# Kernel tuning notes

Hardware: AMD Instinct MI355X
Metric: run time of the kernel (lower is better)

Reference implementation:

```python
import jax, jax.numpy as jnp
import numpy as np

N_NODES = 10000
N_EDGES = 640000
D = 128


def setup_inputs() -> dict:
    key = jax.random.key(0)
    ks = jax.random.split(key, 8)
    x = jax.random.normal(ks[0], (N_NODES, D), dtype=jnp.float32)
    edge_weight = jax.random.uniform(ks[1], (N_EDGES,), dtype=jnp.float32)
    W0 = jax.random.normal(ks[2], (D, D), dtype=jnp.float32) * (1.0 / np.sqrt(D))
    b0 = jnp.zeros((D,), dtype=jnp.float32)
    W1 = jax.random.normal(ks[3], (D, D), dtype=jnp.float32) * (1.0 / np.sqrt(D))
    b1 = jnp.zeros((D,), dtype=jnp.float32)
    src = jax.random.randint(ks[4], (N_EDGES,), 0, N_NODES)
    dst = jax.random.randint(ks[5], (N_EDGES,), 0, N_NODES)
    return {"x": x, "edge_weight": edge_weight, "W0": W0, "b0": b0,
            "W1": W1, "b1": b1, "src": src, "dst": dst}


def _graph_conv(h, src, dst, edge_weight, W, b):
    # DGL GraphConv with norm='both', bias, activation=relu.
    n = h.shape[0]
    ones = jnp.ones((src.shape[0],), dtype=h.dtype)
    out_deg = jax.ops.segment_sum(ones, src, num_segments=n)
    in_deg = jax.ops.segment_sum(ones, dst, num_segments=n)
    norm_src = jax.lax.rsqrt(jnp.maximum(out_deg, 1.0))  # [N]
    norm_dst = jax.lax.rsqrt(jnp.maximum(in_deg, 1.0))   # [N]
    h = h * norm_src[:, None]
    # gather -> weight edges -> scatter-add (sparse neighbor aggregation)
    msg = h[src] * edge_weight[:, None]                  # [E, D]
    agg = jax.ops.segment_sum(msg, dst, num_segments=n)  # [N, D]
    rst = agg @ W                                        # in_feats == out_feats: aggregate first
    rst = rst * norm_dst[:, None] + b
    return jax.nn.relu(rst)  # activation inside GraphConv


def reference(x, edge_weight, W0, b0, W1, b1, src, dst):
    # NET.forward (full-graph path): per layer GraphConv -> activation -> dropout.
    # Dropout is identity in eval mode; outer relu after GraphConv's internal relu is idempotent
    # but applied for faithfulness.
    h = jax.nn.relu(_graph_conv(x, src, dst, edge_weight, W0, b0))
    h = jax.nn.relu(_graph_conv(h, src, dst, edge_weight, W1, b1))
    return h  # predict is None (n_classes=None)
```

## Files before the change

kernel.cpp:

```cpp
#include <hip/hip_runtime.h>
#include <hip/hip_fp16.h>

#define D 128
#define NB 256
#define Q 8
#define BQ (NB / Q)
#define NBINS_MAX 10016
#define GM 32

__global__ __launch_bounds__(256) void cast_kernel(const float* __restrict__ x, __half* __restrict__ xh, int total4) {
    int i = blockIdx.x * 256 + threadIdx.x;
    if (i >= total4) return;
    float4 v = *(const float4*)(x + (size_t)i * 4);
    __half2 a = __floats2half2_rn(v.x, v.y);
    __half2 b = __floats2half2_rn(v.z, v.w);
    *(__half2*)(xh + (size_t)i * 4) = a;
    *(__half2*)(xh + (size_t)i * 4 + 2) = b;
}

__global__ __launch_bounds__(256) void hist_kernel(const int* __restrict__ src, const int* __restrict__ dst,
                                                   int* __restrict__ pd, unsigned short* __restrict__ ps,
                                                   int E, int n) {
    __shared__ __align__(16) int hd[NBINS_MAX];
    __shared__ __align__(16) int hs[NBINS_MAX];
    int b = blockIdx.x, t = threadIdx.x;
    int chunk = (E + NB - 1) / NB;
    int e0 = b * chunk, e1 = min(e0 + chunk, E);
    int nq = (n + 3) >> 2;
    for (int i = t; i < nq; i += 256) {
        *(int4*)(&hd[i * 4]) = make_int4(0, 0, 0, 0);
        *(int4*)(&hs[i * 4]) = make_int4(0, 0, 0, 0);
    }
    __syncthreads();
    for (int e = e0 + t; e < e1; e += 256) {
        atomicAdd(&hd[dst[e]], 1);
        atomicAdd(&hs[src[e]], 1);
    }
    __syncthreads();
    int nf = n >> 2;
    for (int i = t; i < nf; i += 256) {
        int4 h = *(const int4*)(&hd[i * 4]);
        *(int4*)(pd + (size_t)b * n + i * 4) = h;
        int4 s = *(const int4*)(&hs[i * 4]);
        uint2 u;
        u.x = (unsigned)(s.x & 0xFFFF) | ((unsigned)(s.y & 0xFFFF) << 16);
        u.y = (unsigned)(s.z & 0xFFFF) | ((unsigned)(s.w & 0xFFFF) << 16);
        *(uint2*)(ps + (size_t)b * n + i * 4) = u;
    }
    for (int i = nf * 4 + t; i < n; i += 256) {
        pd[(size_t)b * n + i] = hd[i];
        ps[(size_t)b * n + i] = (unsigned short)hs[i];
    }
}

__global__ __launch_bounds__(256) void colscan_kernel(int* __restrict__ pd, const unsigned short* __restrict__ ps,
                                                      int* __restrict__ qtot_d, int* __restrict__ qtot_s, int n) {
    int bin4 = (blockIdx.x * 256 + threadIdx.x) * 4;
    int q = blockIdx.y;
    if (bin4 >= n) return;
    int b0 = q * BQ;
    if (bin4 + 3 < n) {
        int4 run = make_int4(0, 0, 0, 0);
        int4 ssum = make_int4(0, 0, 0, 0);
#pragma unroll 8
        for (int j = 0; j < BQ; ++j) {
            size_t idx = (size_t)(b0 + j) * n + bin4;
            int4 v = *(const int4*)(pd + idx);
            *(int4*)(pd + idx) = run;
            run.x += v.x; run.y += v.y; run.z += v.z; run.w += v.w;
            uint2 u = *(const uint2*)(ps + idx);
            ssum.x += (int)(u.x & 0xFFFF); ssum.y += (int)(u.x >> 16);
            ssum.z += (int)(u.y & 0xFFFF); ssum.w += (int)(u.y >> 16);
        }
        *(int4*)(qtot_d + (size_t)q * n + bin4) = run;
        *(int4*)(qtot_s + (size_t)q * n + bin4) = ssum;
    } else {
        for (int bin = bin4; bin < n; ++bin) {
            int run = 0, ssum = 0;
            for (int j = 0; j < BQ; ++j) {
                size_t idx = (size_t)(b0 + j) * n + bin;
                int v = pd[idx];
                pd[idx] = run;
                run += v;
                ssum += (int)ps[idx];
            }
            qtot_d[(size_t)q * n + bin] = run;
            qtot_s[(size_t)q * n + bin] = ssum;
        }
    }
}

__global__ __launch_bounds__(256) void finalize_kernel(int* __restrict__ qtot_d ,
                                                       const int* __restrict__ qtot_s,
                                                       int* __restrict__ in_deg,
                                                       float* __restrict__ norm_src, float* __restrict__ norm_dst,
                                                       int n) {
    int b4 = (blockIdx.x * 256 + threadIdx.x) * 4;
    if (b4 >= n) return;
    if (b4 + 3 < n) {
        int4 qv[Q];
#pragma unroll
        for (int q = 0; q < Q; ++q) qv[q] = *(const int4*)(qtot_d + (size_t)q * n + b4);
        int4 run = make_int4(0, 0, 0, 0);
#pragma unroll
        for (int q = 0; q < Q; ++q) {
            *(int4*)(qtot_d + (size_t)q * n + b4) = run;
            run.x += qv[q].x; run.y += qv[q].y; run.z += qv[q].z; run.w += qv[q].w;
        }
        *(int4*)(in_deg + b4) = run;
        norm_dst[b4 + 0] = rsqrtf(fmaxf((float)run.x, 1.0f));
        norm_dst[b4 + 1] = rsqrtf(fmaxf((float)run.y, 1.0f));
        norm_dst[b4 + 2] = rsqrtf(fmaxf((float)run.z, 1.0f));
        norm_dst[b4 + 3] = rsqrtf(fmaxf((float)run.w, 1.0f));
        int4 st = make_int4(0, 0, 0, 0);
#pragma unroll
        for (int q = 0; q < Q; ++q) {
            int4 v = *(const int4*)(qtot_s + (size_t)q * n + b4);
            st.x += v.x; st.y += v.y; st.z += v.z; st.w += v.w;
        }
        norm_src[b4 + 0] = rsqrtf(fmaxf((float)st.x, 1.0f));
        norm_src[b4 + 1] = rsqrtf(fmaxf((float)st.y, 1.0f));
        norm_src[b4 + 2] = rsqrtf(fmaxf((float)st.z, 1.0f));
        norm_src[b4 + 3] = rsqrtf(fmaxf((float)st.w, 1.0f));
    } else {
        for (int bin = b4; bin < n; ++bin) {
            int run = 0;
            for (int q = 0; q < Q; ++q) {
                size_t i = (size_t)q * n + bin;
                int v = qtot_d[i];
                qtot_d[i] = run;
                run += v;
            }
            in_deg[bin] = run;
            norm_dst[bin] = rsqrtf(fmaxf((float)run, 1.0f));
            int tot = 0;
            for (int q = 0; q < Q; ++q) tot += qtot_s[(size_t)q * n + bin];
            norm_src[bin] = rsqrtf(fmaxf((float)tot, 1.0f));
        }
    }
}

__global__ __launch_bounds__(1024) void scan_kernel(const int* __restrict__ in_deg, int* __restrict__ row_start, int n) {
    __shared__ int buf[NBINS_MAX];
    __shared__ int part[1024];
    int t = threadIdx.x;
    for (int i = t; i < n; i += 1024) buf[i] = in_deg[i];
    __syncthreads();
    int ipt = (n + 1023) / 1024;
    int lo = min(t * ipt, n), hi = min(lo + ipt, n);
    int s = 0;
    for (int i = lo; i < hi; ++i) s += buf[i];
    part[t] = s;
    __syncthreads();
    for (int off = 1; off < 1024; off <<= 1) {
        int v = 0;
        if (t >= off) v = part[t - off];
        __syncthreads();
        if (t >= off) part[t] += v;
        __syncthreads();
    }
    int run = part[t] - s;
    for (int i = lo; i < hi; ++i) {
        int v = buf[i];
        buf[i] = run;
        run += v;
    }
    __syncthreads();
    for (int i = t; i < n; i += 1024) row_start[i] = buf[i];
    if (t == 0) row_start[n] = part[1023];
}

__global__ __launch_bounds__(256) void fill_kernel(const int* __restrict__ src, const int* __restrict__ dst,
                                                   const float* __restrict__ ew, const float* __restrict__ ns,
                                                   const int* __restrict__ row_start, const int* __restrict__ qbase,
                                                   const int* __restrict__ pd,
                                                   int2* __restrict__ sorted, int E, int n) {
    __shared__ __align__(16) int cursor[NBINS_MAX];
    int b = blockIdx.x, t = threadIdx.x;
    int q = b / BQ;
    int chunk = (E + NB - 1) / NB;
    int e0 = b * chunk, e1 = min(e0 + chunk, E);
    int nf = n >> 2;
    for (int i = t; i < nf; i += 256) {
        int4 r = *(const int4*)(row_start + i * 4);
        int4 a = *(const int4*)(qbase + (size_t)q * n + i * 4);
        int4 c = *(const int4*)(pd + (size_t)b * n + i * 4);
        *(int4*)(&cursor[i * 4]) = make_int4(r.x + a.x + c.x, r.y + a.y + c.y,
                                             r.z + a.z + c.z, r.w + a.w + c.w);
    }
    for (int i = nf * 4 + t; i < n; i += 256)
        cursor[i] = row_start[i] + qbase[(size_t)q * n + i] + pd[(size_t)b * n + i];
    __syncthreads();
    for (int e = e0 + t; e < e1; e += 256) {
        int d = dst[e];
        int slot = atomicAdd(&cursor[d], 1);
        int s = src[e];
        int2 rec;
        rec.x = s;
        rec.y = __float_as_int(ew[e] * ns[s]);
        sorted[slot] = rec;
    }
}

__global__ __launch_bounds__(256) void agg_kernel(const __half* __restrict__ h, const int* __restrict__ row_start,
                                                  const int2* __restrict__ sorted, float* __restrict__ out,
                                                  int n, int qn) {
    int slot  = blockIdx.x & 7;
    int g     = blockIdx.x >> 3;
    int chunk = slot >> 2;
    int quad  = slot & 3;
    int wave  = threadIdx.x >> 6;
    int lane  = threadIdx.x & 63;
    int node  = quad * qn + g * 4 + wave;
    int hiN   = min((quad + 1) * qn, n);
    if (node >= hiN) return;
    const __half* hc = h + chunk * 64 + lane;
    int beg = __builtin_amdgcn_readfirstlane(row_start[node]);
    int end = __builtin_amdgcn_readfirstlane(row_start[node + 1]);
    float acc = 0.f;
    int s = beg;
    if (s < end && (s & 1)) {
        int2 rr = sorted[s];
        acc = fmaf(__int_as_float(rr.y), __half2float(hc[(size_t)rr.x << 7]), acc);
        ++s;
    }
    int4 p0, p1, p2, p3, p4, p5, p6, p7;
    if (s + 16 <= end) {
        p0 = *(const int4*)(sorted + s);
        p1 = *(const int4*)(sorted + s + 2);
        p2 = *(const int4*)(sorted + s + 4);
        p3 = *(const int4*)(sorted + s + 6);
        p4 = *(const int4*)(sorted + s + 8);
        p5 = *(const int4*)(sorted + s + 10);
        p6 = *(const int4*)(sorted + s + 12);
        p7 = *(const int4*)(sorted + s + 14);
    }
    for (; s + 32 <= end; s += 16) {
        int4 q0 = *(const int4*)(sorted + s + 16);
        int4 q1 = *(const int4*)(sorted + s + 18);
        int4 q2 = *(const int4*)(sorted + s + 20);
        int4 q3 = *(const int4*)(sorted + s + 22);
        int4 q4 = *(const int4*)(sorted + s + 24);
        int4 q5 = *(const int4*)(sorted + s + 26);
        int4 q6 = *(const int4*)(sorted + s + 28);
        int4 q7 = *(const int4*)(sorted + s + 30);
        __half x0  = hc[(size_t)p0.x << 7];
        __half x1  = hc[(size_t)p0.z << 7];
        __half x2  = hc[(size_t)p1.x << 7];
        __half x3  = hc[(size_t)p1.z << 7];
        __half x4  = hc[(size_t)p2.x << 7];
        __half x5  = hc[(size_t)p2.z << 7];
        __half x6  = hc[(size_t)p3.x << 7];
        __half x7  = hc[(size_t)p3.z << 7];
        __half x8  = hc[(size_t)p4.x << 7];
        __half x9  = hc[(size_t)p4.z << 7];
        __half x10 = hc[(size_t)p5.x << 7];
        __half x11 = hc[(size_t)p5.z << 7];
        __half x12 = hc[(size_t)p6.x << 7];
        __half x13 = hc[(size_t)p6.z << 7];
        __half x14 = hc[(size_t)p7.x << 7];
        __half x15 = hc[(size_t)p7.z << 7];
        acc = fmaf(__int_as_float(p0.y), __half2float(x0),  acc);
        acc = fmaf(__int_as_float(p0.w), __half2float(x1),  acc);
        acc = fmaf(__int_as_float(p1.y), __half2float(x2),  acc);
        acc = fmaf(__int_as_float(p1.w), __half2float(x3),  acc);
        acc = fmaf(__int_as_float(p2.y), __half2float(x4),  acc);
        acc = fmaf(__int_as_float(p2.w), __half2float(x5),  acc);
        acc = fmaf(__int_as_float(p3.y), __half2float(x6),  acc);
        acc = fmaf(__int_as_float(p3.w), __half2float(x7),  acc);
        acc = fmaf(__int_as_float(p4.y), __half2float(x8),  acc);
        acc = fmaf(__int_as_float(p4.w), __half2float(x9),  acc);
        acc = fmaf(__int_as_float(p5.y), __half2float(x10), acc);
        acc = fmaf(__int_as_float(p5.w), __half2float(x11), acc);
        acc = fmaf(__int_as_float(p6.y), __half2float(x12), acc);
        acc = fmaf(__int_as_float(p6.w), __half2float(x13), acc);
        acc = fmaf(__int_as_float(p7.y), __half2float(x14), acc);
        acc = fmaf(__int_as_float(p7.w), __half2float(x15), acc);
        p0 = q0; p1 = q1; p2 = q2; p3 = q3;
        p4 = q4; p5 = q5; p6 = q6; p7 = q7;
    }
    if (s + 16 <= end) {
        acc = fmaf(__int_as_float(p0.y), __half2float(hc[(size_t)p0.x << 7]), acc);
        acc = fmaf(__int_as_float(p0.w), __half2float(hc[(size_t)p0.z << 7]), acc);
        acc = fmaf(__int_as_float(p1.y), __half2float(hc[(size_t)p1.x << 7]), acc);
        acc = fmaf(__int_as_float(p1.w), __half2float(hc[(size_t)p1.z << 7]), acc);
        acc = fmaf(__int_as_float(p2.y), __half2float(hc[(size_t)p2.x << 7]), acc);
        acc = fmaf(__int_as_float(p2.w), __half2float(hc[(size_t)p2.z << 7]), acc);
        acc = fmaf(__int_as_float(p3.y), __half2float(hc[(size_t)p3.x << 7]), acc);
        acc = fmaf(__int_as_float(p3.w), __half2float(hc[(size_t)p3.z << 7]), acc);
        acc = fmaf(__int_as_float(p4.y), __half2float(hc[(size_t)p4.x << 7]), acc);
        acc = fmaf(__int_as_float(p4.w), __half2float(hc[(size_t)p4.z << 7]), acc);
        acc = fmaf(__int_as_float(p5.y), __half2float(hc[(size_t)p5.x << 7]), acc);
        acc = fmaf(__int_as_float(p5.w), __half2float(hc[(size_t)p5.z << 7]), acc);
        acc = fmaf(__int_as_float(p6.y), __half2float(hc[(size_t)p6.x << 7]), acc);
        acc = fmaf(__int_as_float(p6.w), __half2float(hc[(size_t)p6.z << 7]), acc);
        acc = fmaf(__int_as_float(p7.y), __half2float(hc[(size_t)p7.x << 7]), acc);
        acc = fmaf(__int_as_float(p7.w), __half2float(hc[(size_t)p7.z << 7]), acc);
        s += 16;
    }
    if (s + 8 <= end) {
        int4 a0 = *(const int4*)(sorted + s);
        int4 a1 = *(const int4*)(sorted + s + 2);
        int4 a2 = *(const int4*)(sorted + s + 4);
        int4 a3 = *(const int4*)(sorted + s + 6);
        acc = fmaf(__int_as_float(a0.y), __half2float(hc[(size_t)a0.x << 7]), acc);
        acc = fmaf(__int_as_float(a0.w), __half2float(hc[(size_t)a0.z << 7]), acc);
        acc = fmaf(__int_as_float(a1.y), __half2float(hc[(size_t)a1.x << 7]), acc);
        acc = fmaf(__int_as_float(a1.w), __half2float(hc[(size_t)a1.z << 7]), acc);
        acc = fmaf(__int_as_float(a2.y), __half2float(hc[(size_t)a2.x << 7]), acc);
        acc = fmaf(__int_as_float(a2.w), __half2float(hc[(size_t)a2.z << 7]), acc);
        acc = fmaf(__int_as_float(a3.y), __half2float(hc[(size_t)a3.x << 7]), acc);
        acc = fmaf(__int_as_float(a3.w), __half2float(hc[(size_t)a3.z << 7]), acc);
        s += 8;
    }
    for (; s + 2 <= end; s += 2) {
        int4 p = *(const int4*)(sorted + s);
        acc = fmaf(__int_as_float(p.y), __half2float(hc[(size_t)p.x << 7]), acc);
        acc = fmaf(__int_as_float(p.w), __half2float(hc[(size_t)p.z << 7]), acc);
    }
    if (s < end) {
        int2 rr = sorted[s];
        acc = fmaf(__int_as_float(rr.y), __half2float(hc[(size_t)rr.x << 7]), acc);
    }
    out[((size_t)node << 7) + chunk * 64 + lane] = acc;
}

template <int HALF_OUT>
__global__ __launch_bounds__(256) void gemm_kernel(const float* __restrict__ A, const float* __restrict__ W,
                                                   const float* __restrict__ bias, const float* __restrict__ norm_dst,
                                                   float* __restrict__ out, __half* __restrict__ out_h, int n) {
    __shared__ __align__(16) float sAT[D][GM + 2];
    int tid = threadIdx.x;
    int row0 = blockIdx.x * GM;
    for (int i = tid; i < GM * 32; i += 256) {
        int r = i >> 5;
        int kq = i & 31;
        int rr = row0 + r;
        float4 v = make_float4(0.f, 0.f, 0.f, 0.f);
        if (rr < n) v = *(const float4*)(A + (size_t)rr * D + kq * 4);
        sAT[kq * 4 + 0][r] = v.x;
        sAT[kq * 4 + 1][r] = v.y;
        sAT[kq * 4 + 2][r] = v.z;
        sAT[kq * 4 + 3][r] = v.w;
    }
    __syncthreads();
    int tx = tid & 15;
    int ty = tid >> 4;
    int c0 = tx * 8;
    int r0 = ty * 2;
    float acc0[8], acc1[8];
#pragma unroll
    for (int j = 0; j < 8; ++j) { acc0[j] = 0.f; acc1[j] = 0.f; }
    const float* Wk = W + c0;
#pragma unroll 4
    for (int k = 0; k < D; ++k) {
        float2 a = *(const float2*)&sAT[k][r0];
        float4 w0 = *(const float4*)(Wk);
        float4 w1 = *(const float4*)(Wk + 4);
        Wk += D;
        acc0[0] = fmaf(a.x, w0.x, acc0[0]);
        acc0[1] = fmaf(a.x, w0.y, acc0[1]);
        acc0[2] = fmaf(a.x, w0.z, acc0[2]);
        acc0[3] = fmaf(a.x, w0.w, acc0[3]);
        acc0[4] = fmaf(a.x, w1.x, acc0[4]);
        acc0[5] = fmaf(a.x, w1.y, acc0[5]);
        acc0[6] = fmaf(a.x, w1.z, acc0[6]);
        acc0[7] = fmaf(a.x, w1.w, acc0[7]);
        acc1[0] = fmaf(a.y, w0.x, acc1[0]);
        acc1[1] = fmaf(a.y, w0.y, acc1[1]);
        acc1[2] = fmaf(a.y, w0.z, acc1[2]);
        acc1[3] = fmaf(a.y, w0.w, acc1[3]);
        acc1[4] = fmaf(a.y, w1.x, acc1[4]);
        acc1[5] = fmaf(a.y, w1.y, acc1[5]);
        acc1[6] = fmaf(a.y, w1.z, acc1[6]);
        acc1[7] = fmaf(a.y, w1.w, acc1[7]);
    }
#pragma unroll 2
    for (int rr = 0; rr < 2; ++rr) {
        int r = row0 + r0 + rr;
        if (r >= n) continue;
        float* acc = rr ? acc1 : acc0;
        float nd = norm_dst[r];
        float o[8];
#pragma unroll
        for (int j = 0; j < 8; ++j) o[j] = fmaxf(fmaf(acc[j], nd, bias[c0 + j]), 0.f);
        if (HALF_OUT) {
            __half2 h0 = __floats2half2_rn(o[0], o[1]);
            __half2 h1 = __floats2half2_rn(o[2], o[3]);
            __half2 h2 = __floats2half2_rn(o[4], o[5]);
            __half2 h3 = __floats2half2_rn(o[6], o[7]);
            __half* p = out_h + (size_t)r * D + c0;
            *(__half2*)(p + 0) = h0;
            *(__half2*)(p + 2) = h1;
            *(__half2*)(p + 4) = h2;
            *(__half2*)(p + 6) = h3;
        } else {
            float4 o0 = make_float4(o[0], o[1], o[2], o[3]);
            float4 o1 = make_float4(o[4], o[5], o[6], o[7]);
            *(float4*)(out + (size_t)r * D + c0) = o0;
            *(float4*)(out + (size_t)r * D + c0 + 4) = o1;
        }
    }
}

extern "C" void kernel_launch(void* const* d_in, const int* in_sizes, int n_in,
                              void* d_out, int out_size, void* d_ws, size_t ws_size,
                              hipStream_t stream) {
    const float* x  = (const float*)d_in[0];
    const float* ew = (const float*)d_in[1];
    const float* W0 = (const float*)d_in[2];
    const float* b0 = (const float*)d_in[3];
    const float* W1 = (const float*)d_in[4];
    const float* b1 = (const float*)d_in[5];
    const int* src  = (const int*)d_in[6];
    const int* dst  = (const int*)d_in[7];
    float* out = (float*)d_out;

    int n = in_sizes[0] / D;
    int E = in_sizes[6];
    if (n <= 0 || E <= 0) return;

    char* ws = (char*)d_ws;
    size_t off = 0;
    auto alloc = [&](size_t bytes) -> void* {
        void* p = ws + off;
        off = (off + bytes + 255) & ~(size_t)255;
        return p;
    };
    int* row_start  = (int*)alloc(((size_t)n + 1) * 4);
    int* in_deg     = (int*)alloc((size_t)n * 4);
    float* norm_src = (float*)alloc((size_t)n * 4);
    float* norm_dst = (float*)alloc((size_t)n * 4);
    int* qtot_d     = (int*)alloc((size_t)Q * n * 4);
    int* qtot_s     = (int*)alloc((size_t)Q * n * 4);
    int2* sorted    = (int2*)alloc((size_t)E * 8);
    int* pd         = (int*)alloc((size_t)NB * n * 4);
    unsigned short* ps = (unsigned short*)alloc((size_t)NB * n * 2);
    float* B1       = (float*)alloc((size_t)n * D * 4);
    __half* xh      = (__half*)alloc((size_t)n * D * 2);
    __half* B2h     = (__half*)alloc((size_t)n * D * 2);

    int nb4 = (n + 1023) / 1024;
    int qn = (n + 3) / 4;
    int ab = 8 * ((qn + 3) / 4);
    int gb = (n + GM - 1) / GM;
    int cb = ((n * D / 4) + 255) / 256;

    cast_kernel<<<cb, 256, 0, stream>>>(x, xh, n * D / 4);
    hist_kernel<<<NB, 256, 0, stream>>>(src, dst, pd, ps, E, n);
    colscan_kernel<<<dim3(nb4, Q), 256, 0, stream>>>(pd, ps, qtot_d, qtot_s, n);
    finalize_kernel<<<nb4, 256, 0, stream>>>(qtot_d, qtot_s, in_deg, norm_src, norm_dst, n);
    scan_kernel<<<1, 1024, 0, stream>>>(in_deg, row_start, n);
    fill_kernel<<<NB, 256, 0, stream>>>(src, dst, ew, norm_src, row_start, qtot_d, pd, sorted, E, n);

    agg_kernel<<<ab, 256, 0, stream>>>(xh, row_start, sorted, B1, n, qn);
    gemm_kernel<1><<<gb, 256, 0, stream>>>(B1, W0, b0, norm_dst, nullptr, B2h, n);
    agg_kernel<<<ab, 256, 0, stream>>>(B2h, row_start, sorted, B1, n, qn);
    gemm_kernel<0><<<gb, 256, 0, stream>>>(B1, W1, b1, norm_dst, out, nullptr, n);
}
```

Baseline: 189.4 us.

## Fuse cast into histogram, merge finalize with scan, widen aggregation to half2

Folds the fp32-to-fp16 cast of x into the histogram kernel and merges the finalize and scan kernels into a single 1024-thread block, cutting two launches and the in_deg round-trip. The aggregation kernel now has one wave handle all 128 features of a node using half2 loads, instead of eight blocks splitting each node into 64-column chunks. Each edge record is then read once per node rather than twice, and the gathers are wider. In exchange, finalize work is serialized into one block, and the quad-based node interleaving that may have helped load balance is dropped.

```diff
diff --git a/kernel.cpp b/kernel.cpp
--- a/kernel.cpp
+++ b/kernel.cpp
@@ -8,22 +8,20 @@
 #define NBINS_MAX 10016
 #define GM 32
 
-__global__ __launch_bounds__(256) void cast_kernel(const float* __restrict__ x, __half* __restrict__ xh, int total4) {
-    int i = blockIdx.x * 256 + threadIdx.x;
-    if (i >= total4) return;
-    float4 v = *(const float4*)(x + (size_t)i * 4);
-    __half2 a = __floats2half2_rn(v.x, v.y);
-    __half2 b = __floats2half2_rn(v.z, v.w);
-    *(__half2*)(xh + (size_t)i * 4) = a;
-    *(__half2*)(xh + (size_t)i * 4 + 2) = b;
-}
-
 __global__ __launch_bounds__(256) void hist_kernel(const int* __restrict__ src, const int* __restrict__ dst,
+                                                   const float* __restrict__ x, __half* __restrict__ xh, int total4,
                                                    int* __restrict__ pd, unsigned short* __restrict__ ps,
                                                    int E, int n) {
     __shared__ __align__(16) int hd[NBINS_MAX];
     __shared__ __align__(16) int hs[NBINS_MAX];
     int b = blockIdx.x, t = threadIdx.x;
+    for (int i = b * 256 + t; i < total4; i += NB * 256) {
+        float4 v = *(const float4*)(x + (size_t)i * 4);
+        __half2 a = __floats2half2_rn(v.x, v.y);
+        __half2 c = __floats2half2_rn(v.z, v.w);
+        *(__half2*)(xh + (size_t)i * 4) = a;
+        *(__half2*)(xh + (size_t)i * 4 + 2) = c;
+    }
     int chunk = (E + NB - 1) / NB;
     int e0 = b * chunk, e1 = min(e0 + chunk, E);
     int nq = (n + 3) >> 2;
@@ -90,66 +88,61 @@
     }
 }
 
-__global__ __launch_bounds__(256) void finalize_kernel(int* __restrict__ qtot_d ,
-                                                       const int* __restrict__ qtot_s,
-                                                       int* __restrict__ in_deg,
+__global__ __launch_bounds__(1024) void finscan_kernel(int* __restrict__ qtot_d, const int* __restrict__ qtot_s,
+                                                       int* __restrict__ row_start,
                                                        float* __restrict__ norm_src, float* __restrict__ norm_dst,
                                                        int n) {
-    int b4 = (blockIdx.x * 256 + threadIdx.x) * 4;
-    if (b4 >= n) return;
-    if (b4 + 3 < n) {
-        int4 qv[Q];
-#pragma unroll
-        for (int q = 0; q < Q; ++q) qv[q] = *(const int4*)(qtot_d + (size_t)q * n + b4);
-        int4 run = make_int4(0, 0, 0, 0);
-#pragma unroll
-        for (int q = 0; q < Q; ++q) {
-            *(int4*)(qtot_d + (size_t)q * n + b4) = run;
-            run.x += qv[q].x; run.y += qv[q].y; run.z += qv[q].z; run.w += qv[q].w;
-        }
-        *(int4*)(in_deg + b4) = run;
-        norm_dst[b4 + 0] = rsqrtf(fmaxf((float)run.x, 1.0f));
-        norm_dst[b4 + 1] = rsqrtf(fmaxf((float)run.y, 1.0f));
-        norm_dst[b4 + 2] = rsqrtf(fmaxf((float)run.z, 1.0f));
-        norm_dst[b4 + 3] = rsqrtf(fmaxf((float)run.w, 1.0f));
-        int4 st = make_int4(0, 0, 0, 0);
-#pragma unroll
-        for (int q = 0; q < Q; ++q) {
-            int4 v = *(const int4*)(qtot_s + (size_t)q * n + b4);
-            st.x += v.x; st.y += v.y; st.z += v.z; st.w += v.w;
-        }
-        norm_src[b4 + 0] = rsqrtf(fmaxf((float)st.x, 1.0f));
-        norm_src[b4 + 1] = rsqrtf(fmaxf((float)st.y, 1.0f));
-        norm_src[b4 + 2] = rsqrtf(fmaxf((float)st.z, 1.0f));
-        norm_src[b4 + 3] = rsqrtf(fmaxf((float)st.w, 1.0f));
-    } else {
-        for (int bin = b4; bin < n; ++bin) {
-            int run = 0;
-            for (int q = 0; q < Q; ++q) {
-                size_t i = (size_t)q * n + bin;
-                int v = qtot_d[i];
-                qtot_d[i] = run;
-                run += v;
-            }
-            in_deg[bin] = run;
-            norm_dst[bin] = rsqrtf(fmaxf((float)run, 1.0f));
-            int tot = 0;
-            for (int q = 0; q < Q; ++q) tot += qtot_s[(size_t)q * n + bin];
-            norm_src[bin] = rsqrtf(fmaxf((float)tot, 1.0f));
-        }
-    }
-}
-
-__global__ __launch_bounds__(1024) void scan_kernel(const int* __restrict__ in_deg, int* __restrict__ row_start, int n) {
-    __shared__ int buf[NBINS_MAX];
+    __shared__ int deg[NBINS_MAX];
     __shared__ int part[1024];
     int t = threadIdx.x;
-    for (int i = t; i < n; i += 1024) buf[i] = in_deg[i];
+    for (int b4 = t * 4; b4 < n; b4 += 4096) {
+        if (b4 + 3 < n) {
+            int4 qv[Q];
+#pragma unroll
+            for (int q = 0; q < Q; ++q) qv[q] = *(const int4*)(qtot_d + (size_t)q * n + b4);
+            int4 run = make_int4(0, 0, 0, 0);
+#pragma unroll
+            for (int q = 0; q < Q; ++q) {
+                *(int4*)(qtot_d + (size_t)q * n + b4) = run;
+                run.x += qv[q].x; run.y += qv[q].y; run.z += qv[q].z; run.w += qv[q].w;
+            }
+            *(int4*)(&deg[b4]) = run;
+            norm_dst[b4 + 0] = rsqrtf(fmaxf((float)run.x, 1.0f));
+            norm_dst[b4 + 1] = rsqrtf(fmaxf((float)run.y, 1.0f));
+            norm_dst[b4 + 2] = rsqrtf(fmaxf((float)run.z, 1.0f));
+            norm_dst[b4 + 3] = rsqrtf(fmaxf((float)run.w, 1.0f));
+            int4 st = make_int4(0, 0, 0, 0);
+#pragma unroll
+            for (int q = 0; q < Q; ++q) {
+                int4 v = *(const int4*)(qtot_s + (size_t)q * n + b4);
+                st.x += v.x; st.y += v.y; st.z += v.z; st.w += v.w;
+            }
+            norm_src[b4 + 0] = rsqrtf(fmaxf((float)st.x, 1.0f));
+            norm_src[b4 + 1] = rsqrtf(fmaxf((float)st.y, 1.0f));
+            norm_src[b4 + 2] = rsqrtf(fmaxf((float)st.z, 1.0f));
+            norm_src[b4 + 3] = rsqrtf(fmaxf((float)st.w, 1.0f));
+        } else {
+            for (int bin = b4; bin < n; ++bin) {
+                int run = 0;
+                for (int q = 0; q < Q; ++q) {
+                    size_t i = (size_t)q * n + bin;
+                    int v = qtot_d[i];
+                    qtot_d[i] = run;
+                    run += v;
+                }
+                deg[bin] = run;
+                norm_dst[bin] = rsqrtf(fmaxf((float)run, 1.0f));
+                int tot = 0;
+                for (int q = 0; q < Q; ++q) tot += qtot_s[(size_t)q * n + bin];
+                norm_src[bin] = rsqrtf(fmaxf((float)tot, 1.0f));
+            }
+        }
+    }
     __syncthreads();
     int ipt = (n + 1023) / 1024;
     int lo = min(t * ipt, n), hi = min(lo + ipt, n);
     int s = 0;
-    for (int i = lo; i < hi; ++i) s += buf[i];
+    for (int i = lo; i < hi; ++i) s += deg[i];
     part[t] = s;
     __syncthreads();
     for (int off = 1; off < 1024; off <<= 1) {
@@ -161,13 +154,11 @@
     }
     int run = part[t] - s;
     for (int i = lo; i < hi; ++i) {
-        int v = buf[i];
-        buf[i] = run;
+        int v = deg[i];
+        row_start[i] = run;
         run += v;
     }
-    __syncthreads();
-    for (int i = t; i < n; i += 1024) row_start[i] = buf[i];
-    if (t == 0) row_start[n] = part[1023];
+    if (t == 1023) row_start[n] = part[1023];
 }
 
 __global__ __launch_bounds__(256) void fill_kernel(const int* __restrict__ src, const int* __restrict__ dst,
@@ -203,25 +194,21 @@
 }
 
 __global__ __launch_bounds__(256) void agg_kernel(const __half* __restrict__ h, const int* __restrict__ row_start,
-                                                  const int2* __restrict__ sorted, float* __restrict__ out,
-                                                  int n, int qn) {
-    int slot  = blockIdx.x & 7;
-    int g     = blockIdx.x >> 3;
-    int chunk = slot >> 2;
-    int quad  = slot & 3;
-    int wave  = threadIdx.x >> 6;
-    int lane  = threadIdx.x & 63;
-    int node  = quad * qn + g * 4 + wave;
-    int hiN   = min((quad + 1) * qn, n);
-    if (node >= hiN) return;
-    const __half* hc = h + chunk * 64 + lane;
+                                                  const int2* __restrict__ sorted, float* __restrict__ out, int n) {
+    int wave = threadIdx.x >> 6;
+    int lane = threadIdx.x & 63;
+    int node = blockIdx.x * 4 + wave;
+    if (node >= n) return;
+    const __half2* hc = (const __half2*)h + lane;
     int beg = __builtin_amdgcn_readfirstlane(row_start[node]);
     int end = __builtin_amdgcn_readfirstlane(row_start[node + 1]);
-    float acc = 0.f;
+    float accx = 0.f, accy = 0.f;
     int s = beg;
     if (s < end && (s & 1)) {
         int2 rr = sorted[s];
-        acc = fmaf(__int_as_float(rr.y), __half2float(hc[(size_t)rr.x << 7]), acc);
+        float w = __int_as_float(rr.y);
+        float2 f = __half22float2(hc[(size_t)rr.x << 6]);
+        accx = fmaf(w, f.x, accx); accy = fmaf(w, f.y, accy);
         ++s;
     }
     int4 p0, p1, p2, p3, p4, p5, p6, p7;
@@ -244,58 +231,60 @@
         int4 q5 = *(const int4*)(sorted + s + 26);
         int4 q6 = *(const int4*)(sorted + s + 28);
         int4 q7 = *(const int4*)(sorted + s + 30);
-        __half x0  = hc[(size_t)p0.x << 7];
-        __half x1  = hc[(size_t)p0.z << 7];
-        __half x2  = hc[(size_t)p1.x << 7];
-        __half x3  = hc[(size_t)p1.z << 7];
-        __half x4  = hc[(size_t)p2.x << 7];
-        __half x5  = hc[(size_t)p2.z << 7];
-        __half x6  = hc[(size_t)p3.x << 7];
-        __half x7  = hc[(size_t)p3.z << 7];
-        __half x8  = hc[(size_t)p4.x << 7];
-        __half x9  = hc[(size_t)p4.z << 7];
-        __half x10 = hc[(size_t)p5.x << 7];
-        __half x11 = hc[(size_t)p5.z << 7];
-        __half x12 = hc[(size_t)p6.x << 7];
-        __half x13 = hc[(size_t)p6.z << 7];
-        __half x14 = hc[(size_t)p7.x << 7];
-        __half x15 = hc[(size_t)p7.z << 7];
-        acc = fmaf(__int_as_float(p0.y), __half2float(x0),  acc);
-        acc = fmaf(__int_as_float(p0.w), __half2float(x1),  acc);
-        acc = fmaf(__int_as_float(p1.y), __half2float(x2),  acc);
-        acc = fmaf(__int_as_float(p1.w), __half2float(x3),  acc);
-        acc = fmaf(__int_as_float(p2.y), __half2float(x4),  acc);
-        acc = fmaf(__int_as_float(p2.w), __half2float(x5),  acc);
-        acc = fmaf(__int_as_float(p3.y), __half2float(x6),  acc);
-        acc = fmaf(__int_as_float(p3.w), __half2float(x7),  acc);
-        acc = fmaf(__int_as_float(p4.y), __half2float(x8),  acc);
-        acc = fmaf(__int_as_float(p4.w), __half2float(x9),  acc);
-        acc = fmaf(__int_as_float(p5.y), __half2float(x10), acc);
-        acc = fmaf(__int_as_float(p5.w), __half2float(x11), acc);
-        acc = fmaf(__int_as_float(p6.y), __half2float(x12), acc);
-        acc = fmaf(__int_as_float(p6.w), __half2float(x13), acc);
-        acc = fmaf(__int_as_float(p7.y), __half2float(x14), acc);
-        acc = fmaf(__int_as_float(p7.w), __half2float(x15), acc);
+        __half2 x0  = hc[(size_t)p0.x << 6];
+        __half2 x1  = hc[(size_t)p0.z << 6];
+        __half2 x2  = hc[(size_t)p1.x << 6];
+        __half2 x3  = hc[(size_t)p1.z << 6];
+        __half2 x4  = hc[(size_t)p2.x << 6];
+        __half2 x5  = hc[(size_t)p2.z << 6];
+        __half2 x6  = hc[(size_t)p3.x << 6];
+        __half2 x7  = hc[(size_t)p3.z << 6];
+        __half2 x8  = hc[(size_t)p4.x << 6];
+        __half2 x9  = hc[(size_t)p4.z << 6];
+        __half2 x10 = hc[(size_t)p5.x << 6];
+        __half2 x11 = hc[(size_t)p5.z << 6];
+        __half2 x12 = hc[(size_t)p6.x << 6];
+        __half2 x13 = hc[(size_t)p6.z << 6];
+        __half2 x14 = hc[(size_t)p7.x << 6];
+        __half2 x15 = hc[(size_t)p7.z << 6];
+        float2 f;
+        f = __half22float2(x0);  accx = fmaf(__int_as_float(p0.y), f.x, accx); accy = fmaf(__int_as_float(p0.y), f.y, accy);
+        f = __half22float2(x1);  accx = fmaf(__int_as_float(p0.w), f.x, accx); accy = fmaf(__int_as_float(p0.w), f.y, accy);
+        f = __half22float2(x2);  accx = fmaf(__int_as_float(p1.y), f.x, accx); accy = fmaf(__int_as_float(p1.y), f.y, accy);
+        f = __half22float2(x3);  accx = fmaf(__int_as_float(p1.w), f.x, accx); accy = fmaf(__int_as_float(p1.w), f.y, accy);
+        f = __half22float2(x4);  accx = fmaf(__int_as_float(p2.y), f.x, accx); accy = fmaf(__int_as_float(p2.y), f.y, accy);
+        f = __half22float2(x5);  accx = fmaf(__int_as_float(p2.w), f.x, accx); accy = fmaf(__int_as_float(p2.w), f.y, accy);
+        f = __half22float2(x6);  accx = fmaf(__int_as_float(p3.y), f.x, accx); accy = fmaf(__int_as_float(p3.y), f.y, accy);
+        f = __half22float2(x7);  accx = fmaf(__int_as_float(p3.w), f.x, accx); accy = fmaf(__int_as_float(p3.w), f.y, accy);
+        f = __half22float2(x8);  accx = fmaf(__int_as_float(p4.y), f.x, accx); accy = fmaf(__int_as_float(p4.y), f.y, accy);
+        f = __half22float2(x9);  accx = fmaf(__int_as_float(p4.w), f.x, accx); accy = fmaf(__int_as_float(p4.w), f.y, accy);
+        f = __half22float2(x10); accx = fmaf(__int_as_float(p5.y), f.x, accx); accy = fmaf(__int_as_float(p5.y), f.y, accy);
+        f = __half22float2(x11); accx = fmaf(__int_as_float(p5.w), f.x, accx); accy = fmaf(__int_as_float(p5.w), f.y, accy);
+        f = __half22float2(x12); accx = fmaf(__int_as_float(p6.y), f.x, accx); accy = fmaf(__int_as_float(p6.y), f.y, accy);
+        f = __half22float2(x13); accx = fmaf(__int_as_float(p6.w), f.x, accx); accy = fmaf(__int_as_float(p6.w), f.y, accy);
+        f = __half22float2(x14); accx = fmaf(__int_as_float(p7.y), f.x, accx); accy = fmaf(__int_as_float(p7.y), f.y, accy);
+        f = __half22float2(x15); accx = fmaf(__int_as_float(p7.w), f.x, accx); accy = fmaf(__int_as_float(p7.w), f.y, accy);
         p0 = q0; p1 = q1; p2 = q2; p3 = q3;
         p4 = q4; p5 = q5; p6 = q6; p7 = q7;
     }
     if (s + 16 <= end) {
-        acc = fmaf(__int_as_float(p0.y), __half2float(hc[(size_t)p0.x << 7]), acc);
-        acc = fmaf(__int_as_float(p0.w), __half2float(hc[(size_t)p0.z << 7]), acc);
-        acc = fmaf(__int_as_float(p1.y), __half2float(hc[(size_t)p1.x << 7]), acc);
-        acc = fmaf(__int_as_float(p1.w), __half2float(hc[(size_t)p1.z << 7]), acc);
-        acc = fmaf(__int_as_float(p2.y), __half2float(hc[(size_t)p2.x << 7]), acc);
-        acc = fmaf(__int_as_float(p2.w), __half2float(hc[(size_t)p2.z << 7]), acc);
-        acc = fmaf(__int_as_float(p3.y), __half2float(hc[(size_t)p3.x << 7]), acc);
-        acc = fmaf(__int_as_float(p3.w), __half2float(hc[(size_t)p3.z << 7]), acc);
-        acc = fmaf(__int_as_float(p4.y), __half2float(hc[(size_t)p4.x << 7]), acc);
-        acc = fmaf(__int_as_float(p4.w), __half2float(hc[(size_t)p4.z << 7]), acc);
-        acc = fmaf(__int_as_float(p5.y), __half2float(hc[(size_t)p5.x << 7]), acc);
-        acc = fmaf(__int_as_float(p5.w), __half2float(hc[(size_t)p5.z << 7]), acc);
-        acc = fmaf(__int_as_float(p6.y), __half2float(hc[(size_t)p6.x << 7]), acc);
-        acc = fmaf(__int_as_float(p6.w), __half2float(hc[(size_t)p6.z << 7]), acc);
-        acc = fmaf(__int_as_float(p7.y), __half2float(hc[(size_t)p7.x << 7]), acc);
-        acc = fmaf(__int_as_float(p7.w), __half2float(hc[(size_t)p7.z << 7]), acc);
+        float2 f;
+        f = __half22float2(hc[(size_t)p0.x << 6]); accx = fmaf(__int_as_float(p0.y), f.x, accx); accy = fmaf(__int_as_float(p0.y), f.y, accy);
+        f = __half22float2(hc[(size_t)p0.z << 6]); accx = fmaf(__int_as_float(p0.w), f.x, accx); accy = fmaf(__int_as_float(p0.w), f.y, accy);
+        f = __half22float2(hc[(size_t)p1.x << 6]); accx = fmaf(__int_as_float(p1.y), f.x, accx); accy = fmaf(__int_as_float(p1.y), f.y, accy);
+        f = __half22float2(hc[(size_t)p1.z << 6]); accx = fmaf(__int_as_float(p1.w), f.x, accx); accy = fmaf(__int_as_float(p1.w), f.y, accy);
+        f = __half22float2(hc[(size_t)p2.x << 6]); accx = fmaf(__int_as_float(p2.y), f.x, accx); accy = fmaf(__int_as_float(p2.y), f.y, accy);
+        f = __half22float2(hc[(size_t)p2.z << 6]); accx = fmaf(__int_as_float(p2.w), f.x, accx); accy = fmaf(__int_as_float(p2.w), f.y, accy);
+        f = __half22float2(hc[(size_t)p3.x << 6]); accx = fmaf(__int_as_float(p3.y), f.x, accx); accy = fmaf(__int_as_float(p3.y), f.y, accy);
+        f = __half22float2(hc[(size_t)p3.z << 6]); accx = fmaf(__int_as_float(p3.w), f.x, accx); accy = fmaf(__int_as_float(p3.w), f.y, accy);
+        f = __half22float2(hc[(size_t)p4.x << 6]); accx = fmaf(__int_as_float(p4.y), f.x, accx); accy = fmaf(__int_as_float(p4.y), f.y, accy);
+        f = __half22float2(hc[(size_t)p4.z << 6]); accx = fmaf(__int_as_float(p4.w), f.x, accx); accy = fmaf(__int_as_float(p4.w), f.y, accy);
+        f = __half22float2(hc[(size_t)p5.x << 6]); accx = fmaf(__int_as_float(p5.y), f.x, accx); accy = fmaf(__int_as_float(p5.y), f.y, accy);
+        f = __half22float2(hc[(size_t)p5.z << 6]); accx = fmaf(__int_as_float(p5.w), f.x, accx); accy = fmaf(__int_as_float(p5.w), f.y, accy);
+        f = __half22float2(hc[(size_t)p6.x << 6]); accx = fmaf(__int_as_float(p6.y), f.x, accx); accy = fmaf(__int_as_float(p6.y), f.y, accy);
+        f = __half22float2(hc[(size_t)p6.z << 6]); accx = fmaf(__int_as_float(p6.w), f.x, accx); accy = fmaf(__int_as_float(p6.w), f.y, accy);
+        f = __half22float2(hc[(size_t)p7.x << 6]); accx = fmaf(__int_as_float(p7.y), f.x, accx); accy = fmaf(__int_as_float(p7.y), f.y, accy);
+        f = __half22float2(hc[(size_t)p7.z << 6]); accx = fmaf(__int_as_float(p7.w), f.x, accx); accy = fmaf(__int_as_float(p7.w), f.y, accy);
         s += 16;
     }
     if (s + 8 <= end) {
@@ -303,26 +292,31 @@
         int4 a1 = *(const int4*)(sorted + s + 2);
         int4 a2 = *(const int4*)(sorted + s + 4);
         int4 a3 = *(const int4*)(sorted + s + 6);
-        acc = fmaf(__int_as_float(a0.y), __half2float(hc[(size_t)a0.x << 7]), acc);
-        acc = fmaf(__int_as_float(a0.w), __half2float(hc[(size_t)a0.z << 7]), acc);
-        acc = fmaf(__int_as_float(a1.y), __half2float(hc[(size_t)a1.x << 7]), acc);
-        acc = fmaf(__int_as_float(a1.w), __half2float(hc[(size_t)a1.z << 7]), acc);
-        acc = fmaf(__int_as_float(a2.y), __half2float(hc[(size_t)a2.x << 7]), acc);
-        acc = fmaf(__int_as_float(a2.w), __half2float(hc[(size_t)a2.z << 7]), acc);
-        acc = fmaf(__int_as_float(a3.y), __half2float(hc[(size_t)a3.x << 7]), acc);
-        acc = fmaf(__int_as_float(a3.w), __half2float(hc[(size_t)a3.z << 7]), acc);
+        float2 f;
+        f = __half22float2(hc[(size_t)a0.x << 6]); accx = fmaf(__int_as_float(a0.y), f.x, accx); accy = fmaf(__int_as_float(a0.y), f.y, accy);
+        f = __half22float2(hc[(size_t)a0.z << 6]); accx = fmaf(__int_as_float(a0.w), f.x, accx); accy = fmaf(__int_as_float(a0.w), f.y, accy);
+        f = __half22float2(hc[(size_t)a1.x << 6]); accx = fmaf(__int_as_float(a1.y), f.x, accx); accy = fmaf(__int_as_float(a1.y), f.y, accy);
+        f = __half22float2(hc[(size_t)a1.z << 6]); accx = fmaf(__int_as_float(a1.w), f.x, accx); accy = fmaf(__int_as_float(a1.w), f.y, accy);
+        f = __half22float2(hc[(size_t)a2.x << 6]); accx = fmaf(__int_as_float(a2.y), f.x, accx); accy = fmaf(__int_as_float(a2.y), f.y, accy);
+        f = __half22float2(hc[(size_t)a2.z << 6]); accx = fmaf(__int_as_float(a2.w), f.x, accx); accy = fmaf(__int_as_float(a2.w), f.y, accy);
+        f = __half22float2(hc[(size_t)a3.x << 6]); accx = fmaf(__int_as_float(a3.y), f.x, accx); accy = fmaf(__int_as_float(a3.y), f.y, accy);
+        f = __half22float2(hc[(size_t)a3.z << 6]); accx = fmaf(__int_as_float(a3.w), f.x, accx); accy = fmaf(__int_as_float(a3.w), f.y, accy);
         s += 8;
     }
     for (; s + 2 <= end; s += 2) {
         int4 p = *(const int4*)(sorted + s);
-        acc = fmaf(__int_as_float(p.y), __half2float(hc[(size_t)p.x << 7]), acc);
-        acc = fmaf(__int_as_float(p.w), __half2float(hc[(size_t)p.z << 7]), acc);
+        float2 f;
+        f = __half22float2(hc[(size_t)p.x << 6]); accx = fmaf(__int_as_float(p.y), f.x, accx); accy = fmaf(__int_as_float(p.y), f.y, accy);
+        f = __half22float2(hc[(size_t)p.z << 6]); accx = fmaf(__int_as_float(p.w), f.x, accx); accy = fmaf(__int_as_float(p.w), f.y, accy);
     }
     if (s < end) {
         int2 rr = sorted[s];
-        acc = fmaf(__int_as_float(rr.y), __half2float(hc[(size_t)rr.x << 7]), acc);
-    }
-    out[((size_t)node << 7) + chunk * 64 + lane] = acc;
+        float w = __int_as_float(rr.y);
+        float2 f = __half22float2(hc[(size_t)rr.x << 6]);
+        accx = fmaf(w, f.x, accx); accy = fmaf(w, f.y, accy);
+    }
+    float2 o; o.x = accx; o.y = accy;
+    *(float2*)(out + ((size_t)node << 7) + lane * 2) = o;
 }
 
 template <int HALF_OUT>
@@ -428,7 +422,6 @@
         return p;
     };
     int* row_start  = (int*)alloc(((size_t)n + 1) * 4);
-    int* in_deg     = (int*)alloc((size_t)n * 4);
     float* norm_src = (float*)alloc((size_t)n * 4);
     float* norm_dst = (float*)alloc((size_t)n * 4);
     int* qtot_d     = (int*)alloc((size_t)Q * n * 4);
@@ -441,20 +434,16 @@
     __half* B2h     = (__half*)alloc((size_t)n * D * 2);
 
     int nb4 = (n + 1023) / 1024;
-    int qn = (n + 3) / 4;
-    int ab = 8 * ((qn + 3) / 4);
+    int ab = (n + 3) / 4;
     int gb = (n + GM - 1) / GM;
-    int cb = ((n * D / 4) + 255) / 256;
-
-    cast_kernel<<<cb, 256, 0, stream>>>(x, xh, n * D / 4);
-    hist_kernel<<<NB, 256, 0, stream>>>(src, dst, pd, ps, E, n);
+
+    hist_kernel<<<NB, 256, 0, stream>>>(src, dst, x, xh, n * D / 4, pd, ps, E, n);
     colscan_kernel<<<dim3(nb4, Q), 256, 0, stream>>>(pd, ps, qtot_d, qtot_s, n);
-    finalize_kernel<<<nb4, 256, 0, stream>>>(qtot_d, qtot_s, in_deg, norm_src, norm_dst, n);
-    scan_kernel<<<1, 1024, 0, stream>>>(in_deg, row_start, n);
+    finscan_kernel<<<1, 1024, 0, stream>>>(qtot_d, qtot_s, row_start, norm_src, norm_dst, n);
     fill_kernel<<<NB, 256, 0, stream>>>(src, dst, ew, norm_src, row_start, qtot_d, pd, sorted, E, n);
 
-    agg_kernel<<<ab, 256, 0, stream>>>(xh, row_start, sorted, B1, n, qn);
+    agg_kernel<<<ab, 256, 0, stream>>>(xh, row_start, sorted, B1, n);
     gemm_kernel<1><<<gb, 256, 0, stream>>>(B1, W0, b0, norm_dst, nullptr, B2h, n);
-    agg_kernel<<<ab, 256, 0, stream>>>(B2h, row_start, sorted, B1, n, qn);
+    agg_kernel<<<ab, 256, 0, stream>>>(B2h, row_start, sorted, B1, n);
     gemm_kernel<0><<<gb, 256, 0, stream>>>(B1, W1, b1, norm_dst, out, nullptr, n);
 }
```

After: 186.5 us. Within noise of the previous version (-1.5%).
